# Kernel tuning notes

Hardware: AMD Instinct MI355X
Metric: run time of the kernel (lower is better)

Reference implementation:

```python
import jax, jax.numpy as jnp
import numpy as np

N_EMBED = 1024
N_HEAD = 64  # head (value) dimension, per source: Linear(n_embed, n_head)
B = 8
C = 2048


def setup_inputs() -> dict:
    key = jax.random.key(0)
    k1, k2, k3, k4, k5 = jax.random.split(key, 5)
    bound = 1.0 / np.sqrt(N_EMBED)  # torch Linear default init range
    x = jax.random.normal(k1, (B, C, N_EMBED), dtype=jnp.float32)
    Wq = jax.random.uniform(k2, (N_EMBED, N_HEAD), dtype=jnp.float32, minval=-bound, maxval=bound)
    Wk = jax.random.uniform(k3, (N_EMBED, N_HEAD), dtype=jnp.float32, minval=-bound, maxval=bound)
    Wv = jax.random.uniform(k4, (N_EMBED, N_HEAD), dtype=jnp.float32, minval=-bound, maxval=bound)
    zero_mask = jax.random.randint(k5, (B, C), 0, 2) == 1
    return {"x": x, "Wq": Wq, "Wk": Wk, "Wv": Wv, "zero_mask": zero_mask}


def reference(x, Wq, Wk, Wv, zero_mask):
    # x: [B, C, n_embed]; zero_mask: [B, C] bool (zeroes whole query rows post-softmax)
    Bc, Cc, _ = x.shape
    q = x @ Wq  # [B, C, H]
    k = x @ Wk
    v = x @ Wv
    # NOTE: source scales by C**-0.5 (sequence length), not head_dim**-0.5
    scores = jnp.einsum('bqh,bkh->bqk', q, k) * (float(Cc) ** -0.5)  # [B, C, C]
    causal = jnp.tril(jnp.ones((Cc, Cc), dtype=bool))
    scores = jnp.where(causal[None], scores, -jnp.inf)
    a = jax.nn.softmax(scores, axis=-1)
    a = jnp.where(zero_mask[..., None], jnp.zeros((), dtype=a.dtype), a)  # post-softmax zero mask
    return a @ v  # [B, C, H]
```

## Files before the change

### kernel.cpp

```cpp
#include <hip/hip_runtime.h>
#include <math.h>


#define B_ 8
#define C_ 2048
#define E_ 1024
#define H_ 64
#define SCALE 0.02209708691207961f

typedef __attribute__((ext_vector_type(8))) short short8;
typedef __attribute__((ext_vector_type(4))) float floatx4;

union BF8 { short8 s8; unsigned int u[4]; };

static __device__ __forceinline__ unsigned int pack_bf2(float lo, float hi) {
    unsigned int a = __builtin_bit_cast(unsigned int, lo);
    unsigned int b = __builtin_bit_cast(unsigned int, hi);
    return (a >> 16) | (b & 0xFFFF0000u);
}
static __device__ __forceinline__ unsigned short f2bf(float f) {
    return (unsigned short)(__builtin_bit_cast(unsigned int, f) >> 16);
}
static __device__ __forceinline__ void load_lds16(const void* g, void* l) {
    __builtin_amdgcn_global_load_lds(
        (const __attribute__((address_space(1))) void*)g,
        (__attribute__((address_space(3))) void*)l, 16, 0, 0);
}

__global__ __launch_bounds__(256) void wcvt_kernel(
    const float* __restrict__ Wq, const float* __restrict__ Wk,
    const float* __restrict__ Wv, unsigned short* __restrict__ wt)
{
    __shared__ float lds[64][68];
    const int bid = (int)blockIdx.x;
    const int m = bid >> 4, kt = bid & 15, k0 = kt * 64;
    const float* W = (m == 0) ? Wq : (m == 1) ? Wk : Wv;
    const int t = (int)threadIdx.x;
#pragma unroll
    for (int j = 0; j < 4; j++) {
        int idx4 = j * 256 + t;
        int row = idx4 >> 4, c4 = idx4 & 15;
        float4 v = *(const float4*)(W + (size_t)(k0 + row) * 64 + c4 * 4);
        *(float4*)&lds[row][c4 * 4] = v;
    }
    __syncthreads();
#pragma unroll
    for (int j = 0; j < 2; j++) {
        int g = j * 256 + t;
        int n = g >> 3, kk = (g & 7) * 8;
        unsigned int o[4];
#pragma unroll
        for (int i = 0; i < 4; i++)
            o[i] = pack_bf2(lds[kk + 2 * i][n], lds[kk + 2 * i + 1][n]);
        *(uint4*)(wt + (size_t)(m * 64 + n) * 1024 + k0 + kk) =
            make_uint4(o[0], o[1], o[2], o[3]);
    }
}

__global__ __launch_bounds__(256, 2) void qkv_kernel(
    const float* __restrict__ X, const unsigned short* __restrict__ wt,
    unsigned short* __restrict__ qg, unsigned short* __restrict__ kg,
    unsigned short* __restrict__ vtile)
{
    __shared__ __align__(16) unsigned char smem[3 * 8192 + 2 * 24576];
    unsigned short* vstage = (unsigned short*)smem;

    const int t = (int)threadIdx.x;
    const int w = t >> 6, lane = t & 63;
    const int l15 = lane & 15, quad = lane >> 4;
    const int r0 = (int)blockIdx.x * 32;
    const int ncol0 = (w & 1) * 96;
    const int rbase = (w >> 1) * 16;

    const int xgi0 = w * 128 + lane;
    const int xr_a = xgi0 >> 4, xs_a = xgi0 & 15;
    const int xg_a = xs_a ^ (xr_a & 15);
    const int xr_b = (xgi0 + 64) >> 4, xs_b = xgi0 & 15;
    const int xg_b = xs_b ^ (xr_b & 15);
    const int wrow_off = lane >> 3, wgs = lane & 7;

    floatx4 acc[6];
#pragma unroll
    for (int j = 0; j < 6; j++) acc[j] = (floatx4){0.f, 0.f, 0.f, 0.f};

#define STAGE_X(c, q) do {                                                   \
        load_lds16(X + (size_t)(r0 + xr_a) * E_ + (c) * 64 + xg_a * 4,       \
                   smem + (q) * 8192 + (w * 128) * 16);                      \
        load_lds16(X + (size_t)(r0 + xr_b) * E_ + (c) * 64 + xg_b * 4,       \
                   smem + (q) * 8192 + (w * 128 + 64) * 16);                 \
    } while (0)
#define STAGE_W(c, q) do {                                                   \
        _Pragma("unroll")                                                    \
        for (int j = 0; j < 6; j++) {                                        \
            const int region = w * 6 + j;                                    \
            const int row = region * 8 + wrow_off;                           \
            const int gsrc = wgs ^ (row & 7);                                \
            load_lds16(wt + (size_t)row * 1024 + (c) * 64 + gsrc * 8,        \
                       smem + 24576 + (q) * 24576 + region * 1024);          \
        }                                                                    \
    } while (0)

    STAGE_X(0, 0);
    STAGE_X(1, 1);
    STAGE_W(0, 0);

#pragma unroll
    for (int c = 0; c < 16; c++) {
        __syncthreads();
        if (c + 2 < 16) STAGE_X(c + 2, (c + 2) % 3);
        if (c + 1 < 16) STAGE_W(c + 1, (c + 1) & 1);

        const float4* xc = (const float4*)(smem + (c % 3) * 8192);
        const unsigned short* wc =
            (const unsigned short*)(smem + 24576 + (c & 1) * 24576);

#pragma unroll
        for (int ks = 0; ks < 2; ks++) {
            const int g0 = ks * 8 + quad * 2;
            const float4* xrow = xc + (rbase + l15) * 16;
            float4 f0 = xrow[g0 ^ l15];
            float4 f1 = xrow[(g0 + 1) ^ l15];
            BF8 a;
            a.u[0] = pack_bf2(f0.x, f0.y);
            a.u[1] = pack_bf2(f0.z, f0.w);
            a.u[2] = pack_bf2(f1.x, f1.y);
            a.u[3] = pack_bf2(f1.z, f1.w);
#pragma unroll
            for (int nt = 0; nt < 6; nt++) {
                const int n = ncol0 + nt * 16 + l15;
                const int slot = (ks * 4 + quad) ^ (n & 7);
                short8 bfr = *(const short8*)(wc + n * 64 + slot * 8);
                acc[nt] = __builtin_amdgcn_mfma_f32_16x16x32_bf16(
                    a.s8, bfr, acc[nt], 0, 0, 0);
            }
        }
    }
#undef STAGE_X
#undef STAGE_W

    __syncthreads();
    const int bb = r0 >> 11;
    const int keybase = r0 & 2047;
    const int rowl0 = rbase + quad * 4;
#pragma unroll
    for (int nt = 0; nt < 6; nt++) {
        const int n = ncol0 + nt * 16 + l15;
        if (n < 64) {
#pragma unroll
            for (int r = 0; r < 4; r++)
                qg[(size_t)(r0 + rowl0 + r) * 64 + n] = f2bf(acc[nt][r] * SCALE);
        } else if (n < 128) {
#pragma unroll
            for (int r = 0; r < 4; r++)
                kg[(size_t)(r0 + rowl0 + r) * 64 + (n - 64)] = f2bf(acc[nt][r]);
        } else {
            const int h = n - 128;
            *(unsigned int*)&vstage[h * 40 + rowl0] =
                pack_bf2(acc[nt][0], acc[nt][1]);
            *(unsigned int*)&vstage[h * 40 + rowl0 + 2] =
                pack_bf2(acc[nt][2], acc[nt][3]);
        }
    }
    __syncthreads();
    {
        const int h = t >> 2, part = t & 3;
        uint4 v = *(const uint4*)&vstage[h * 40 + part * 8];
        *(uint4*)(vtile + ((size_t)(bb * 32 + (keybase >> 6)) * 64 + h) * 64
                  + (keybase & 63) + part * 8) = v;
    }
}

__global__ __launch_bounds__(128, 2) void attn_kernel(
    const unsigned short* __restrict__ qg, const unsigned short* __restrict__ kg,
    const unsigned short* __restrict__ vtile, const int* __restrict__ zmask,
    float* __restrict__ opart, float* __restrict__ lpart,
    float* __restrict__ out)
{
    __shared__ unsigned short Klds[2][64 * 64];
    __shared__ unsigned short Vlds[2][64 * 64];
    __shared__ unsigned short Ps[2 * 16 * 88];

    const int t = (int)threadIdx.x;
    const int w = t >> 6, lane = t & 63;
    const int l15 = lane & 15, quad = lane >> 4;
    const int b = (int)blockIdx.x;
    const int qt = (int)blockIdx.y;
    const int z = (int)blockIdx.z;
    const int q0 = qt * 32;
    const int nkt = (q0 >> 6) + 1;
    const int t0 = z * 8;
    const int t1 = (t0 + 8 < nkt) ? (t0 + 8) : nkt;
    if (t0 >= t1) return;
    const int ns = (nkt + 7) >> 3;

    const int qlo = q0 + w * 16;
    const int myrow = qlo + quad * 4;
    const int srow_off = lane >> 3, sgs = lane & 7;

    short8 qfr[2];
#pragma unroll
    for (int kc = 0; kc < 2; kc++)
        qfr[kc] = *(const short8*)(qg + ((size_t)b * C_ + qlo + l15) * 64
                                   + kc * 32 + quad * 8);

    floatx4 accO[4];
#pragma unroll
    for (int i = 0; i < 4; i++) accO[i] = (floatx4){0.f, 0.f, 0.f, 0.f};
    float lsum[4] = {0.f, 0.f, 0.f, 0.f};

#pragma unroll
    for (int j = 0; j < 4; j++) {
        const int region = w * 4 + j;
        const int row = region * 8 + srow_off;
        const int gsrc = sgs ^ (row & 7);
        load_lds16(kg + ((size_t)b * C_ + t0 * 64 + row) * 64 + gsrc * 8,
                   &Klds[0][region * 512]);
        load_lds16(vtile + (((size_t)b * 32 + t0) * 64 + row) * 64 + gsrc * 8,
                   &Vlds[0][region * 512]);
    }

    int buf = 0;
    for (int kt = t0; kt < t1; kt++) {
        __syncthreads();
        if (kt + 1 < t1) {
            const int k0n = (kt + 1) * 64;
#pragma unroll
            for (int j = 0; j < 4; j++) {
                const int region = w * 4 + j;
                const int row = region * 8 + srow_off;
                const int gsrc = sgs ^ (row & 7);
                load_lds16(kg + ((size_t)b * C_ + k0n + row) * 64 + gsrc * 8,
                           &Klds[buf ^ 1][region * 512]);
                load_lds16(vtile + (((size_t)b * 32 + kt + 1) * 64 + row) * 64 + gsrc * 8,
                           &Vlds[buf ^ 1][region * 512]);
            }
        }

        floatx4 s[4];
#pragma unroll
        for (int nt = 0; nt < 4; nt++) {
            const int row = nt * 16 + l15;
            short8 kf0 = *(const short8*)&Klds[buf][row * 64 + ((quad) ^ (row & 7)) * 8];
            short8 kf1 = *(const short8*)&Klds[buf][row * 64 + ((4 + quad) ^ (row & 7)) * 8];
            floatx4 zz = (floatx4){0.f, 0.f, 0.f, 0.f};
            zz = __builtin_amdgcn_mfma_f32_16x16x32_bf16(qfr[0], kf0, zz, 0, 0, 0);
            s[nt] = __builtin_amdgcn_mfma_f32_16x16x32_bf16(qfr[1], kf1, zz, 0, 0, 0);
        }
        float pr[4][4];
#pragma unroll
        for (int nt = 0; nt < 4; nt++)
#pragma unroll
            for (int r = 0; r < 4; r++) pr[nt][r] = __expf(s[nt][r]);
        if (kt == nkt - 1) {
            const int k0 = kt * 64;
#pragma unroll
            for (int nt = 0; nt < 4; nt++) {
                const int key = k0 + nt * 16 + l15;
#pragma unroll
                for (int r = 0; r < 4; r++)
                    if (key > myrow + r) pr[nt][r] = 0.f;
            }
        }
#pragma unroll
        for (int nt = 0; nt < 4; nt++)
#pragma unroll
            for (int r = 0; r < 4; r++) {
                lsum[r] += pr[nt][r];
                Ps[(w * 16 + quad * 4 + r) * 88 + nt * 16 + l15] = f2bf(pr[nt][r]);
            }
#pragma unroll
        for (int kc = 0; kc < 2; kc++) {
            short8 af = *(const short8*)&Ps[(w * 16 + l15) * 88 + kc * 32 + quad * 8];
#pragma unroll
            for (int nt = 0; nt < 4; nt++) {
                const int row = nt * 16 + l15;
                short8 vf = *(const short8*)&Vlds[buf][row * 64
                                + ((kc * 4 + quad) ^ (row & 7)) * 8];
                accO[nt] = __builtin_amdgcn_mfma_f32_16x16x32_bf16(
                    af, vf, accO[nt], 0, 0, 0);
            }
        }
        buf ^= 1;
    }

#pragma unroll
    for (int r = 0; r < 4; r++) {
        float v = lsum[r];
        v += __shfl_xor(v, 1);
        v += __shfl_xor(v, 2);
        v += __shfl_xor(v, 4);
        v += __shfl_xor(v, 8);
        lsum[r] = v;
    }

    if (ns == 1) {
        float inv[4];
#pragma unroll
        for (int r = 0; r < 4; r++) {
            int zm = zmask[b * C_ + myrow + r];
            inv[r] = zm ? 0.f : 1.0f / lsum[r];
        }
#pragma unroll
        for (int nt = 0; nt < 4; nt++)
#pragma unroll
            for (int r = 0; r < 4; r++)
                out[(size_t)(b * C_ + myrow + r) * 64 + nt * 16 + l15] =
                    accO[nt][r] * inv[r];
    } else {
        const int lrow = myrow - 512;
        float* ob = opart + ((size_t)(z * 8 + b) * 1536 + lrow) * 64;
#pragma unroll
        for (int nt = 0; nt < 4; nt++)
#pragma unroll
            for (int r = 0; r < 4; r++)
                ob[(size_t)r * 64 + nt * 16 + l15] = accO[nt][r];
        if (l15 == 0) {
#pragma unroll
            for (int r = 0; r < 4; r++)
                lpart[(size_t)(z * 8 + b) * 1536 + lrow + r] = lsum[r];
        }
    }
}

__global__ __launch_bounds__(256) void combine_kernel(
    const float* __restrict__ opart, const float* __restrict__ lpart,
    const int* __restrict__ zmask, float* __restrict__ out)
{
    const int b = (int)blockIdx.y;
    const int gid = (int)blockIdx.x * 256 + (int)threadIdx.x;
    const int lrow = gid >> 4;
    const int f4 = gid & 15;
    const int row = 512 + lrow;
    const int nkt = (row >> 6) + 1;
    const int ns = (nkt + 7) >> 3;

    float4 o = make_float4(0.f, 0.f, 0.f, 0.f);
    float l = 0.f;
    for (int zc = 0; zc < ns; zc++) {
        float4 p = *(const float4*)(opart
            + ((size_t)(zc * 8 + b) * 1536 + lrow) * 64 + f4 * 4);
        o.x += p.x; o.y += p.y; o.z += p.z; o.w += p.w;
        l += lpart[(size_t)(zc * 8 + b) * 1536 + lrow];
    }
    const float inv = zmask[b * C_ + row] ? 0.f : 1.0f / l;
    *(float4*)(out + (size_t)(b * C_ + row) * 64 + f4 * 4) =
        make_float4(o.x * inv, o.y * inv, o.z * inv, o.w * inv);
}

extern "C" void kernel_launch(void* const* d_in, const int* in_sizes, int n_in,
                              void* d_out, int out_size, void* d_ws, size_t ws_size,
                              hipStream_t stream) {
    const float* X  = (const float*)d_in[0];
    const float* Wq = (const float*)d_in[1];
    const float* Wk = (const float*)d_in[2];
    const float* Wv = (const float*)d_in[3];
    const int*   zm = (const int*)d_in[4];
    float* out = (float*)d_out;

    unsigned short* qg    = (unsigned short*)d_ws;
    unsigned short* kg    = qg    + (size_t)B_ * C_ * H_;
    unsigned short* vtile = kg    + (size_t)B_ * C_ * H_;
    unsigned short* wt    = vtile + (size_t)B_ * C_ * H_;
    float* opart = (float*)(wt + (size_t)192 * 1024);
    float* lpart = opart + (size_t)4 * 8 * 1536 * 64;

    wcvt_kernel<<<dim3(48), dim3(256), 0, stream>>>(Wq, Wk, Wv, wt);
    qkv_kernel<<<dim3(512), dim3(256), 0, stream>>>(X, wt, qg, kg, vtile);
    attn_kernel<<<dim3(B_, 64, 4), dim3(128), 0, stream>>>(
        qg, kg, vtile, zm, opart, lpart, out);
    combine_kernel<<<dim3(96, B_), dim3(256), 0, stream>>>(opart, lpart, zm, out);
}
```

Before: 138.7 us.

## Split QKV projection columns across two blocks and shrink LDS staging

The QKV projection grid becomes 512x2. Each block computes 96 of the 192 output columns (Q+K half, or K+V half), and each wave now covers 16 rows by 48 columns. LDS drops to double buffers for both X and W, and launch bounds rise to 4 blocks per CU, which aims at more occupancy and more blocks to spread the load. The cost is that X is read from global memory twice, once per column half, and the X prefetch depth falls from three buffers to two.

```diff
diff --git a/kernel.cpp b/kernel.cpp
--- a/kernel.cpp
+++ b/kernel.cpp
@@ -57,62 +57,64 @@
     }
 }
 
-__global__ __launch_bounds__(256, 2) void qkv_kernel(
+__global__ __launch_bounds__(256, 4) void qkv_kernel(
     const float* __restrict__ X, const unsigned short* __restrict__ wt,
     unsigned short* __restrict__ qg, unsigned short* __restrict__ kg,
     unsigned short* __restrict__ vtile)
 {
-    __shared__ __align__(16) unsigned char smem[3 * 8192 + 2 * 24576];
+    __shared__ __align__(16) unsigned char smem[2 * 8192 + 2 * 12288];
     unsigned short* vstage = (unsigned short*)smem;
 
     const int t = (int)threadIdx.x;
     const int w = t >> 6, lane = t & 63;
     const int l15 = lane & 15, quad = lane >> 4;
     const int r0 = (int)blockIdx.x * 32;
-    const int ncol0 = (w & 1) * 96;
-    const int rbase = (w >> 1) * 16;
-
-    const int xgi0 = w * 128 + lane;
-    const int xr_a = xgi0 >> 4, xs_a = xgi0 & 15;
-    const int xg_a = xs_a ^ (xr_a & 15);
-    const int xr_b = (xgi0 + 64) >> 4, xs_b = xgi0 & 15;
-    const int xg_b = xs_b ^ (xr_b & 15);
+    const int ch = (int)blockIdx.y;
+    const int rbase = (w & 1) * 16;
+    const int nloc0 = (w >> 1) * 48;
+
     const int wrow_off = lane >> 3, wgs = lane & 7;
 
-    floatx4 acc[6];
-#pragma unroll
-    for (int j = 0; j < 6; j++) acc[j] = (floatx4){0.f, 0.f, 0.f, 0.f};
-
+    floatx4 acc[3];
+#pragma unroll
+    for (int j = 0; j < 3; j++) acc[j] = (floatx4){0.f, 0.f, 0.f, 0.f};
+
+#define XBUF(q) (smem + (q) * 8192)
+#define WBUF(q) (smem + 16384 + (q) * 12288)
 #define STAGE_X(c, q) do {                                                   \
-        load_lds16(X + (size_t)(r0 + xr_a) * E_ + (c) * 64 + xg_a * 4,       \
-                   smem + (q) * 8192 + (w * 128) * 16);                      \
-        load_lds16(X + (size_t)(r0 + xr_b) * E_ + (c) * 64 + xg_b * 4,       \
-                   smem + (q) * 8192 + (w * 128 + 64) * 16);                 \
+        _Pragma("unroll")                                                    \
+        for (int j = 0; j < 2; j++) {                                        \
+            const int gi = w * 128 + j * 64 + lane;                          \
+            const int row = gi >> 4;                                         \
+            const int g = (gi & 15) ^ (row & 15);                            \
+            load_lds16(X + (size_t)(r0 + row) * E_ + (c) * 64 + g * 4,       \
+                       XBUF(q) + (w * 128 + j * 64) * 16);                   \
+        }                                                                    \
     } while (0)
 #define STAGE_W(c, q) do {                                                   \
         _Pragma("unroll")                                                    \
-        for (int j = 0; j < 6; j++) {                                        \
-            const int region = w * 6 + j;                                    \
-            const int row = region * 8 + wrow_off;                           \
-            const int gsrc = wgs ^ (row & 7);                                \
-            load_lds16(wt + (size_t)row * 1024 + (c) * 64 + gsrc * 8,        \
-                       smem + 24576 + (q) * 24576 + region * 1024);          \
+        for (int j = 0; j < 3; j++) {                                        \
+            const int region = w * 3 + j;                                    \
+            const int nloc = region * 8 + wrow_off;                          \
+            const int gsrc = wgs ^ (nloc & 7);                               \
+            load_lds16(wt + (size_t)(ch * 96 + nloc) * 1024 + (c) * 64       \
+                          + gsrc * 8,                                        \
+                       WBUF(q) + region * 1024);                             \
         }                                                                    \
     } while (0)
 
     STAGE_X(0, 0);
-    STAGE_X(1, 1);
     STAGE_W(0, 0);
 
 #pragma unroll
     for (int c = 0; c < 16; c++) {
         __syncthreads();
-        if (c + 2 < 16) STAGE_X(c + 2, (c + 2) % 3);
-        if (c + 1 < 16) STAGE_W(c + 1, (c + 1) & 1);
-
-        const float4* xc = (const float4*)(smem + (c % 3) * 8192);
-        const unsigned short* wc =
-            (const unsigned short*)(smem + 24576 + (c & 1) * 24576);
+        if (c + 1 < 16) {
+            STAGE_X(c + 1, (c + 1) & 1);
+            STAGE_W(c + 1, (c + 1) & 1);
+        }
+        const float4* xc = (const float4*)XBUF(c & 1);
+        const unsigned short* wc = (const unsigned short*)WBUF(c & 1);
 
 #pragma unroll
         for (int ks = 0; ks < 2; ks++) {
@@ -126,10 +128,10 @@
             a.u[2] = pack_bf2(f1.x, f1.y);
             a.u[3] = pack_bf2(f1.z, f1.w);
 #pragma unroll
-            for (int nt = 0; nt < 6; nt++) {
-                const int n = ncol0 + nt * 16 + l15;
-                const int slot = (ks * 4 + quad) ^ (n & 7);
-                short8 bfr = *(const short8*)(wc + n * 64 + slot * 8);
+            for (int nt = 0; nt < 3; nt++) {
+                const int nloc = nloc0 + nt * 16 + l15;
+                const int slot = (ks * 4 + quad) ^ (nloc & 7);
+                short8 bfr = *(const short8*)(wc + nloc * 64 + slot * 8);
                 acc[nt] = __builtin_amdgcn_mfma_f32_16x16x32_bf16(
                     a.s8, bfr, acc[nt], 0, 0, 0);
             }
@@ -137,14 +139,16 @@
     }
 #undef STAGE_X
 #undef STAGE_W
-
-    __syncthreads();
+#undef XBUF
+#undef WBUF
+
     const int bb = r0 >> 11;
     const int keybase = r0 & 2047;
     const int rowl0 = rbase + quad * 4;
-#pragma unroll
-    for (int nt = 0; nt < 6; nt++) {
-        const int n = ncol0 + nt * 16 + l15;
+    __syncthreads();
+#pragma unroll
+    for (int nt = 0; nt < 3; nt++) {
+        const int n = ch * 96 + nloc0 + nt * 16 + l15;
         if (n < 64) {
 #pragma unroll
             for (int r = 0; r < 4; r++)
@@ -161,8 +165,8 @@
                 pack_bf2(acc[nt][2], acc[nt][3]);
         }
     }
-    __syncthreads();
-    {
+    if (ch == 1) {
+        __syncthreads();
         const int h = t >> 2, part = t & 3;
         uint4 v = *(const uint4*)&vstage[h * 40 + part * 8];
         *(uint4*)(vtile + ((size_t)(bb * 32 + (keybase >> 6)) * 64 + h) * 64
@@ -365,7 +369,7 @@
     float* lpart = opart + (size_t)4 * 8 * 1536 * 64;
 
     wcvt_kernel<<<dim3(48), dim3(256), 0, stream>>>(Wq, Wk, Wv, wt);
-    qkv_kernel<<<dim3(512), dim3(256), 0, stream>>>(X, wt, qg, kg, vtile);
+    qkv_kernel<<<dim3(512, 2), dim3(256), 0, stream>>>(X, wt, qg, kg, vtile);
     attn_kernel<<<dim3(B_, 64, 4), dim3(128), 0, stream>>>(
         qg, kg, vtile, zm, opart, lpart, out);
     combine_kernel<<<dim3(96, B_), dim3(256), 0, stream>>>(opart, lpart, zm, out);
```

Result: no change. 138.5 us (-0.2%).
